# Kernel optimization log

Measured on AMD Instinct MI355X. Metric: run time of the kernel, lower is better.

## Reference

```python
import jax, jax.numpy as jnp
import numpy as np

UNITS = 1024
N_CLASS = 1024
D_IN = 1024


def setup_inputs() -> dict:
    key = jax.random.key(0)
    ks = jax.random.split(key, 12)
    B, T = 128, 256
    s_in = 1.0 / np.sqrt(D_IN)
    s_h = 1.0 / np.sqrt(UNITS)
    return {
        "x": jax.random.normal(ks[0], (B, T, D_IN), jnp.float32),
        "h0": jax.random.normal(ks[1], (B, UNITS), jnp.float32),
        "c0": jax.random.normal(ks[2], (B, UNITS), jnp.float32),
        "Wk": jax.random.normal(ks[3], (D_IN, 4 * UNITS), jnp.float32) * s_in,
        "bk": jnp.zeros((4 * UNITS,), jnp.float32),
        "Wr": jax.random.normal(ks[4], (UNITS, 4 * UNITS), jnp.float32) * s_h,
        "br": jnp.zeros((4 * UNITS,), jnp.float32),
        "alpha": jax.random.normal(ks[5], (1, 4 * UNITS), jnp.float32) * 0.1,
        "beta1": jax.random.normal(ks[6], (1, 4 * UNITS), jnp.float32) * 0.1,
        "beta2": jax.random.normal(ks[7], (1, 4 * UNITS), jnp.float32) * 0.1,
        "Wc": jax.random.normal(ks[8], (UNITS, N_CLASS), jnp.float32) * s_h,
        "bc": jnp.zeros((N_CLASS,), jnp.float32),
    }


def reference(x, h0, c0, Wk, bk, Wr, br, alpha, beta1, beta2, Wc, bc):
    # x: [B, T, D_in]; scan over time (steps) with MI-LSTM cell
    def step(carry, x_t):
        h, c = carry
        xp = x_t @ Wk + bk          # [B, 4U] input projection
        hp = h @ Wr + br            # [B, 4U] recurrent projection
        z = alpha * xp * hp + beta1 * xp + beta2 * hp  # multiplicative integration
        i, f, g, o = jnp.split(z, 4, axis=1)
        c_new = jnp.tanh(g) * jax.nn.sigmoid(i) + c * jax.nn.sigmoid(f)
        h_new = jnp.tanh(c_new) * jax.nn.sigmoid(o)
        return (h_new, c_new), None

    xs = jnp.transpose(x, (1, 0, 2))  # [T, B, D_in]
    (h, c), _ = jax.lax.scan(step, (h0, c0), xs)
    out = h @ Wc + bc  # [B, n_class]
    return out, h, c
```

## Files before the change

kernel.cpp:

```cpp
#include <hip/hip_runtime.h>


typedef unsigned short u16;
typedef __attribute__((ext_vector_type(8))) short short8;
typedef __attribute__((ext_vector_type(4))) float f32x4;

#define B_SZ   128
#define T_SZ   256
#define D_IN   1024
#define UNITS  1024
#define FOURU  4096

__device__ __forceinline__ float bf2f(u16 h) {
    return __uint_as_float(((unsigned int)h) << 16);
}
__device__ __forceinline__ u16 f2bf(float f) {
    unsigned int u = __float_as_uint(f);
    u += 0x7fffu + ((u >> 16) & 1u);
    return (u16)(u >> 16);
}
__device__ __forceinline__ float sigmoidf_(float x) {
    return 1.0f / (1.0f + __expf(-x));
}

__global__ __launch_bounds__(256) void transpose_cvt(
    const float* __restrict__ in, u16* __restrict__ out, int K, int N)
{
    __shared__ u16 t[32][33];
    int n0 = blockIdx.x * 32, k0 = blockIdx.y * 32;
    int c = threadIdx.x & 31, r = threadIdx.x >> 5;
    #pragma unroll
    for (int i = 0; i < 4; ++i) {
        int kk = r + i * 8;
        t[kk][c] = f2bf(in[(size_t)(k0 + kk) * N + n0 + c]);
    }
    __syncthreads();
    #pragma unroll
    for (int i = 0; i < 4; ++i) {
        int nn = r + i * 8;
        out[(size_t)(n0 + nn) * K + k0 + c] = t[c][nn];
    }
}

__global__ __launch_bounds__(256) void gemm_xp_chunk(
    const float* __restrict__ X, const u16* __restrict__ Bt,
    const float* __restrict__ bias, u16* __restrict__ Cc,
    int t0, int tcShift)
{
    __shared__ __align__(16) u16 As[128 * 40];
    __shared__ __align__(16) u16 Bs[128 * 40];
    int tid = threadIdx.x;
    int wave = tid >> 6, lane = tid & 63;
    int bm = blockIdx.x * 128;
    int bn = blockIdx.y * 128;
    int wm = (wave & 1) * 64, wn = (wave >> 1) * 64;
    int lm = lane & 15, lq = lane >> 4;
    int tcMask = (1 << tcShift) - 1;

    f32x4 acc[4][4] = {};

    for (int k0 = 0; k0 < D_IN; k0 += 32) {
        #pragma unroll
        for (int i = 0; i < 2; ++i) {
            int idx = tid + i * 256;
            int r = idx >> 2, q = idx & 3;
            int rowp = bm + r;
            int b = rowp >> tcShift;
            int tt = rowp & tcMask;
            const float* xs = &X[(size_t)(b * T_SZ + t0 + tt) * D_IN + k0 + q * 8];
            float4 f0 = *(const float4*)xs;
            float4 f1 = *(const float4*)(xs + 4);
            uint4 v;
            v.x = (unsigned)f2bf(f0.x) | ((unsigned)f2bf(f0.y) << 16);
            v.y = (unsigned)f2bf(f0.z) | ((unsigned)f2bf(f0.w) << 16);
            v.z = (unsigned)f2bf(f1.x) | ((unsigned)f2bf(f1.y) << 16);
            v.w = (unsigned)f2bf(f1.z) | ((unsigned)f2bf(f1.w) << 16);
            *(uint4*)&As[r * 40 + q * 8] = v;
            *(uint4*)&Bs[r * 40 + q * 8] =
                *(const uint4*)&Bt[(size_t)(bn + r) * D_IN + k0 + q * 8];
        }
        __syncthreads();
        short8 af[4], bf[4];
        #pragma unroll
        for (int t = 0; t < 4; ++t) {
            af[t] = *(const short8*)&As[(wm + t * 16 + lm) * 40 + lq * 8];
            bf[t] = *(const short8*)&Bs[(wn + t * 16 + lm) * 40 + lq * 8];
        }
        #pragma unroll
        for (int mt = 0; mt < 4; ++mt)
            #pragma unroll
            for (int nt = 0; nt < 4; ++nt)
                acc[mt][nt] = __builtin_amdgcn_mfma_f32_16x16x32_bf16(
                    af[mt], bf[nt], acc[mt][nt], 0, 0, 0);
        __syncthreads();
    }

    #pragma unroll
    for (int mt = 0; mt < 4; ++mt) {
        #pragma unroll
        for (int nt = 0; nt < 4; ++nt) {
            int col = bn + wn + nt * 16 + lm;
            float bv = bias[col];
            #pragma unroll
            for (int r = 0; r < 4; ++r) {
                int rowp = bm + wm + mt * 16 + lq * 4 + r;
                Cc[(size_t)rowp * FOURU + col] = f2bf(acc[mt][nt][r] + bv);
            }
        }
    }
}

__global__ __launch_bounds__(256) void milstm_chunk(
    const u16* __restrict__ XPc,
    const u16* __restrict__ WrT,
    const float* __restrict__ br,
    const float* __restrict__ alpha,
    const float* __restrict__ beta1,
    const float* __restrict__ beta2,
    const u16* __restrict__ h0bf,
    u16* __restrict__ hb0,
    u16* __restrict__ hb1,
    float* __restrict__ cbuf,
    unsigned* __restrict__ bar,
    int t0, int tc, int nbase)
{
    __shared__ __align__(16) u16 WrS[64 * 1032];
    __shared__ float zbuf[2][64][34];
    __shared__ float brS[64], alS[64], b1S[64], b2S[64];

    int tid = threadIdx.x;
    int wave = tid >> 6, lane = tid & 63;
    int lm = lane & 15, lq = lane >> 4;
    int mw = wave & 1, kh = wave >> 1;
    int bid = blockIdx.x;
    int grp = bid >> 6, grp0 = grp * 32;
    int u0 = (bid & 63) * 16;
    unsigned grpBase = (unsigned)grp * 256u;
    unsigned sub = ((unsigned)(bid & 63)) >> 4;

    for (int i = 0; i < 32; ++i) {
        int idx = i * 256 + tid;
        int l = idx >> 7, q = idx & 127;
        int n = ((l >> 4) << 10) + u0 + (l & 15);
        *(uint4*)&WrS[l * 1032 + q * 8] = *(const uint4*)&WrT[(size_t)n * 1024 + q * 8];
    }
    if (tid < 64) {
        int n = ((tid >> 4) << 10) + u0 + (tid & 15);
        brS[tid] = br[n]; alS[tid] = alpha[n];
        b1S[tid] = beta1[n]; b2S[tid] = beta2[n];
    }

    int rl = tid >> 3, j0 = (tid & 7) * 2;
    int bg = grp0 + rl;
    size_t cix = (size_t)bg * UNITS + u0 + j0;
    float cvl[2];
    { float2 c2 = *(const float2*)&cbuf[cix]; cvl[0] = c2.x; cvl[1] = c2.y; }
    __syncthreads();

    unsigned xpq[4];
    {
        const u16* xb = XPc + (size_t)(bg * tc) * FOURU + u0 + j0;
        #pragma unroll
        for (int g = 0; g < 4; ++g) xpq[g] = *(const unsigned*)(xb + (g << 10));
    }

    for (int s = 0; s < tc; ++s) {
        int t = t0 + s;
        const u16* hsrc = (t == 0) ? h0bf : ((t & 1) ? hb0 : hb1);
        u16* hdst = (t & 1) ? hb1 : hb0;

        unsigned long long* Ap = (unsigned long long*)
            &hsrc[(size_t)(grp0 + mw * 16 + lm) * UNITS + kh * 512 + lq * 8];
        unsigned long long aq[32];
        #pragma unroll
        for (int i = 0; i < 16; ++i) {
            aq[2 * i]     = __hip_atomic_load(Ap + i * 8,     __ATOMIC_RELAXED, __HIP_MEMORY_SCOPE_AGENT);
            aq[2 * i + 1] = __hip_atomic_load(Ap + i * 8 + 1, __ATOMIC_RELAXED, __HIP_MEMORY_SCOPE_AGENT);
        }

        const u16* Bl = &WrS[kh * 512 + lq * 8];
        f32x4 acc0 = {}, acc1 = {}, acc2 = {}, acc3 = {};
        #pragma unroll
        for (int i = 0; i < 16; ++i) {
            int k0 = i * 32;
            union { unsigned long long q[2]; short8 v; } a;
            a.q[0] = aq[2 * i]; a.q[1] = aq[2 * i + 1];
            short8 b0 = *(const short8*)&Bl[(0 * 16 + lm) * 1032 + k0];
            short8 b1 = *(const short8*)&Bl[(1 * 16 + lm) * 1032 + k0];
            short8 b2 = *(const short8*)&Bl[(2 * 16 + lm) * 1032 + k0];
            short8 b3 = *(const short8*)&Bl[(3 * 16 + lm) * 1032 + k0];
            acc0 = __builtin_amdgcn_mfma_f32_16x16x32_bf16(a.v, b0, acc0, 0, 0, 0);
            acc1 = __builtin_amdgcn_mfma_f32_16x16x32_bf16(a.v, b1, acc1, 0, 0, 0);
            acc2 = __builtin_amdgcn_mfma_f32_16x16x32_bf16(a.v, b2, acc2, 0, 0, 0);
            acc3 = __builtin_amdgcn_mfma_f32_16x16x32_bf16(a.v, b3, acc3, 0, 0, 0);
        }
        #pragma unroll
        for (int r = 0; r < 4; ++r) {
            int mrow = mw * 16 + lq * 4 + r;
            zbuf[kh][0 * 16 + lm][mrow] = acc0[r];
            zbuf[kh][1 * 16 + lm][mrow] = acc1[r];
            zbuf[kh][2 * 16 + lm][mrow] = acc2[r];
            zbuf[kh][3 * 16 + lm][mrow] = acc3[r];
        }
        __syncthreads();

        float hnew[2];
        #pragma unroll
        for (int jj = 0; jj < 2; ++jj) {
            float zz[4];
            #pragma unroll
            for (int g = 0; g < 4; ++g) {
                int l = g * 16 + j0 + jj;
                float hp = zbuf[0][l][rl] + zbuf[1][l][rl] + brS[l];
                float xp = bf2f((u16)(jj ? (xpq[g] >> 16) : (xpq[g] & 0xffffu)));
                zz[g] = alS[l] * xp * hp + b1S[l] * xp + b2S[l] * hp;
            }
            float cn = tanhf(zz[2]) * sigmoidf_(zz[0]) + cvl[jj] * sigmoidf_(zz[1]);
            cvl[jj] = cn;
            hnew[jj] = tanhf(cn) * sigmoidf_(zz[3]);
        }
        unsigned pk = (unsigned)f2bf(hnew[0]) | ((unsigned)f2bf(hnew[1]) << 16);
        __hip_atomic_store((unsigned*)&hdst[cix], pk,
                           __ATOMIC_RELAXED, __HIP_MEMORY_SCOPE_AGENT);

        if (s + 1 < tc) {
            {
                const u16* xb = XPc + (size_t)(bg * tc + s + 1) * FOURU + u0 + j0;
                #pragma unroll
                for (int g = 0; g < 4; ++g) xpq[g] = *(const unsigned*)(xb + (g << 10));
            }
            unsigned barId = (unsigned)(nbase + s + 1);
            __syncthreads();
            if (tid == 0) {
                unsigned old = __hip_atomic_fetch_add(&bar[grpBase + sub * 32u], 1u,
                                   __ATOMIC_RELAXED, __HIP_MEMORY_SCOPE_AGENT);
                if (old == 16u * barId - 1u)
                    __hip_atomic_fetch_add(&bar[grpBase + 128u], 1u,
                        __ATOMIC_RELAXED, __HIP_MEMORY_SCOPE_AGENT);
                while (__hip_atomic_load(&bar[grpBase + 128u],
                           __ATOMIC_RELAXED, __HIP_MEMORY_SCOPE_AGENT)
                       < 4u * barId)
                    __builtin_amdgcn_s_sleep(2);
            }
            __syncthreads();
        }
    }

    { float2 c2; c2.x = cvl[0]; c2.y = cvl[1]; *(float2*)&cbuf[cix] = c2; }
}

__global__ __launch_bounds__(256) void gemm_out(
    const u16* __restrict__ h, const u16* __restrict__ WcT,
    const float* __restrict__ bc, float* __restrict__ out)
{
    int tid = threadIdx.x;
    int wave = tid >> 6, lane = tid & 63;
    int bx = blockIdx.x;
    int row0 = (bx & 7) * 16;
    int n0 = (bx >> 3) * 64 + wave * 16;
    int lm = lane & 15, lq = lane >> 4;

    f32x4 acc = {};
    const u16* Arow = &h[(size_t)(row0 + lm) * UNITS];
    const u16* Brow = &WcT[(size_t)(n0 + lm) * UNITS];
    #pragma unroll 8
    for (int k0 = 0; k0 < UNITS; k0 += 32) {
        short8 a = *(const short8*)&Arow[k0 + lq * 8];
        short8 b = *(const short8*)&Brow[k0 + lq * 8];
        acc = __builtin_amdgcn_mfma_f32_16x16x32_bf16(a, b, acc, 0, 0, 0);
    }
    int col = n0 + lm;
    float bv = bc[col];
    #pragma unroll
    for (int r = 0; r < 4; ++r) {
        int row = row0 + lq * 4 + r;
        out[(size_t)row * 1024 + col] = acc[r] + bv;
    }
}

__global__ void cvt_f32_bf16(const float* __restrict__ in, u16* __restrict__ out, int n) {
    int i = blockIdx.x * 256 + threadIdx.x;
    if (i < n) out[i] = f2bf(in[i]);
}
__global__ void cvt_bf16_f32(const u16* __restrict__ in, float* __restrict__ out, int n) {
    int i = blockIdx.x * 256 + threadIdx.x;
    if (i < n) out[i] = bf2f(in[i]);
}
__global__ void copy_f32(const float* __restrict__ in, float* __restrict__ out, int n) {
    int i = blockIdx.x * 256 + threadIdx.x;
    if (i < n) out[i] = in[i];
}
__global__ void zero_u32(unsigned* __restrict__ p, int n) {
    int i = blockIdx.x * 256 + threadIdx.x;
    if (i < n) p[i] = 0u;
}

extern "C" void kernel_launch(void* const* d_in, const int* in_sizes, int n_in,
                              void* d_out, int out_size, void* d_ws, size_t ws_size,
                              hipStream_t stream)
{
    const float* x     = (const float*)d_in[0];
    const float* h0    = (const float*)d_in[1];
    const float* c0    = (const float*)d_in[2];
    const float* Wk    = (const float*)d_in[3];
    const float* bk    = (const float*)d_in[4];
    const float* Wr    = (const float*)d_in[5];
    const float* br    = (const float*)d_in[6];
    const float* alpha = (const float*)d_in[7];
    const float* beta1 = (const float*)d_in[8];
    const float* beta2 = (const float*)d_in[9];
    const float* Wc    = (const float*)d_in[10];
    const float* bc    = (const float*)d_in[11];
    float* out = (float*)d_out;

    char* p = (char*)d_ws;
    u16* h0bf = (u16*)p;  p += (size_t)B_SZ * UNITS * 2;
    u16* hb0  = (u16*)p;  p += (size_t)B_SZ * UNITS * 2;
    u16* hb1  = (u16*)p;  p += (size_t)B_SZ * UNITS * 2;
    float* cbuf = (float*)p; p += (size_t)B_SZ * UNITS * 4;
    unsigned* bar = (unsigned*)p; p += 4096;
    u16* WkT = (u16*)p;   p += (size_t)FOURU * D_IN * 2;
    u16* WrT = (u16*)p;   p += (size_t)FOURU * UNITS * 2;
    u16* WcT = (u16*)p;   p += (size_t)1024 * 1024 * 2;
    u16* XPc = (u16*)p;

    size_t fixedB = (size_t)(p - (char*)d_ws);
    int tc = 32, tcShift = 5;
    while (tc > 1 && fixedB + (size_t)B_SZ * tc * FOURU * 2 > ws_size) {
        tc >>= 1; tcShift -= 1;
    }

    transpose_cvt<<<dim3(FOURU / 32, D_IN / 32), 256, 0, stream>>>(Wk, WkT, D_IN, FOURU);
    transpose_cvt<<<dim3(FOURU / 32, UNITS / 32), 256, 0, stream>>>(Wr, WrT, UNITS, FOURU);
    transpose_cvt<<<dim3(1024 / 32, 1024 / 32), 256, 0, stream>>>(Wc, WcT, 1024, 1024);

    cvt_f32_bf16<<<(B_SZ * UNITS) / 256, 256, 0, stream>>>(h0, h0bf, B_SZ * UNITS);
    copy_f32<<<(B_SZ * UNITS) / 256, 256, 0, stream>>>(c0, cbuf, B_SZ * UNITS);
    zero_u32<<<4, 256, 0, stream>>>(bar, 1024);

    for (int t0 = 0; t0 < T_SZ; t0 += tc) {
        gemm_xp_chunk<<<dim3(tc, FOURU / 128), 256, 0, stream>>>(
            x, WkT, bk, XPc, t0, tcShift);
        int nbase = (t0 / tc) * (tc - 1);
        milstm_chunk<<<256, 256, 0, stream>>>(
            XPc, WrT, br, alpha, beta1, beta2, h0bf, hb0, hb1, cbuf, bar,
            t0, tc, nbase);
    }

    gemm_out<<<128, 256, 0, stream>>>(hb1, WcT, bc, out);
    cvt_bf16_f32<<<(B_SZ * UNITS) / 256, 256, 0, stream>>>(hb1, out + B_SZ * UNITS, B_SZ * UNITS);
    copy_f32<<<(B_SZ * UNITS) / 256, 256, 0, stream>>>(cbuf, out + 2 * B_SZ * UNITS, B_SZ * UNITS);
}
```

Baseline: 2.512 ms.

## Split recurrent blocks into two independent 16-row halves with per-half barriers

```diff
diff --git a/kernel.cpp b/kernel.cpp
--- a/kernel.cpp
+++ b/kernel.cpp
@@ -2,6 +2,7 @@
 
 
 typedef unsigned short u16;
+typedef unsigned long long u64t;
 typedef __attribute__((ext_vector_type(8))) short short8;
 typedef __attribute__((ext_vector_type(4))) float f32x4;
 
@@ -100,17 +101,19 @@
         #pragma unroll
         for (int nt = 0; nt < 4; ++nt) {
             int col = bn + wn + nt * 16 + lm;
+            int g = col >> 10, w = col & 1023;
+            int colp = ((w >> 4) << 6) + ((w & 15) << 2) + g;
             float bv = bias[col];
             #pragma unroll
             for (int r = 0; r < 4; ++r) {
                 int rowp = bm + wm + mt * 16 + lq * 4 + r;
-                Cc[(size_t)rowp * FOURU + col] = f2bf(acc[mt][nt][r] + bv);
-            }
-        }
-    }
-}
-
-__global__ __launch_bounds__(256) void milstm_chunk(
+                Cc[(size_t)rowp * FOURU + colp] = f2bf(acc[mt][nt][r] + bv);
+            }
+        }
+    }
+}
+
+__global__ __launch_bounds__(512) void milstm_chunk(
     const u16* __restrict__ XPc,
     const u16* __restrict__ WrT,
     const float* __restrict__ br,
@@ -124,129 +127,169 @@
     unsigned* __restrict__ bar,
     int t0, int tc, int nbase)
 {
-    __shared__ __align__(16) u16 WrS[64 * 1032];
-    __shared__ float zbuf[2][64][34];
+    __shared__ __align__(16) u16 WrS[64 * 1024];
+    __shared__ float zbuf[2][2][64][17];
     __shared__ float brS[64], alS[64], b1S[64], b2S[64];
+    __shared__ unsigned hsync[2];
+    __shared__ unsigned hflag[2];
 
     int tid = threadIdx.x;
-    int wave = tid >> 6, lane = tid & 63;
+    int bid = blockIdx.x;
+    int u_idx = bid & 63, gpair = bid >> 6;
+    int u0 = u_idx * 16;
+    int half = tid >> 8;
+    int x = tid & 255;
+    int kq = x >> 6;
+    int lane = tid & 63;
     int lm = lane & 15, lq = lane >> 4;
-    int mw = wave & 1, kh = wave >> 1;
-    int bid = blockIdx.x;
-    int grp = bid >> 6, grp0 = grp * 32;
-    int u0 = (bid & 63) * 16;
-    unsigned grpBase = (unsigned)grp * 256u;
-    unsigned sub = ((unsigned)(bid & 63)) >> 4;
-
-    for (int i = 0; i < 32; ++i) {
-        int idx = i * 256 + tid;
+    int grpRow0 = gpair * 32 + half * 16;
+    int group = gpair * 2 + half;
+    unsigned gBase = (unsigned)group * 256u;
+    unsigned sub = (unsigned)(u_idx >> 4);
+
+    #pragma unroll
+    for (int it = 0; it < 16; ++it) {
+        int idx = it * 512 + tid;
         int l = idx >> 7, q = idx & 127;
         int n = ((l >> 4) << 10) + u0 + (l & 15);
-        *(uint4*)&WrS[l * 1032 + q * 8] = *(const uint4*)&WrT[(size_t)n * 1024 + q * 8];
+        int byte = l * 2048 + ((q * 16) ^ ((l & 7) << 4));
+        *(uint4*)((char*)WrS + byte) = *(const uint4*)&WrT[(size_t)n * 1024 + q * 8];
     }
     if (tid < 64) {
         int n = ((tid >> 4) << 10) + u0 + (tid & 15);
         brS[tid] = br[n]; alS[tid] = alpha[n];
         b1S[tid] = beta1[n]; b2S[tid] = beta2[n];
     }
-
-    int rl = tid >> 3, j0 = (tid & 7) * 2;
-    int bg = grp0 + rl;
-    size_t cix = (size_t)bg * UNITS + u0 + j0;
-    float cvl[2];
-    { float2 c2 = *(const float2*)&cbuf[cix]; cvl[0] = c2.x; cvl[1] = c2.y; }
+    if (tid < 2) { hsync[tid] = 0u; hflag[tid] = 0u; }
+
+    int ej = x & 15, em = x >> 4;
+    int erow = grpRow0 + em;
+    size_t hixE = (size_t)erow * UNITS + u0 + ej;
+    float cv = cbuf[hixE];
+    u64t xq = *(const u64t*)&XPc[(size_t)(erow * tc) * FOURU + (u_idx << 6) + (ej << 2)];
     __syncthreads();
 
-    unsigned xpq[4];
-    {
-        const u16* xb = XPc + (size_t)(bg * tc) * FOURU + u0 + j0;
-        #pragma unroll
-        for (int g = 0; g < 4; ++g) xpq[g] = *(const unsigned*)(xb + (g << 10));
-    }
+    unsigned st = 0;
+    volatile unsigned* cnt = &hsync[half];
 
     for (int s = 0; s < tc; ++s) {
         int t = t0 + s;
         const u16* hsrc = (t == 0) ? h0bf : ((t & 1) ? hb0 : hb1);
         u16* hdst = (t & 1) ? hb1 : hb0;
 
-        unsigned long long* Ap = (unsigned long long*)
-            &hsrc[(size_t)(grp0 + mw * 16 + lm) * UNITS + kh * 512 + lq * 8];
-        unsigned long long aq[32];
-        #pragma unroll
-        for (int i = 0; i < 16; ++i) {
-            aq[2 * i]     = __hip_atomic_load(Ap + i * 8,     __ATOMIC_RELAXED, __HIP_MEMORY_SCOPE_AGENT);
-            aq[2 * i + 1] = __hip_atomic_load(Ap + i * 8 + 1, __ATOMIC_RELAXED, __HIP_MEMORY_SCOPE_AGENT);
-        }
-
-        const u16* Bl = &WrS[kh * 512 + lq * 8];
+        const u64t* A0 = (const u64t*)
+            &hsrc[(size_t)(grpRow0 + lm) * UNITS + kq * 256 + lq * 8];
+        u64t aq[16];
+        #pragma unroll
+        for (int i = 0; i < 8; ++i) {
+            aq[2 * i]     = __hip_atomic_load(A0 + i * 8,     __ATOMIC_RELAXED, __HIP_MEMORY_SCOPE_AGENT);
+            aq[2 * i + 1] = __hip_atomic_load(A0 + i * 8 + 1, __ATOMIC_RELAXED, __HIP_MEMORY_SCOPE_AGENT);
+        }
+
         f32x4 acc0 = {}, acc1 = {}, acc2 = {}, acc3 = {};
-        #pragma unroll
-        for (int i = 0; i < 16; ++i) {
-            int k0 = i * 32;
-            union { unsigned long long q[2]; short8 v; } a;
+        const char* Wb = (const char*)WrS;
+        int swz = (lm & 7) << 4;
+        #pragma unroll
+        for (int i = 0; i < 8; ++i) {
+            union { u64t q[2]; short8 v; } a;
             a.q[0] = aq[2 * i]; a.q[1] = aq[2 * i + 1];
-            short8 b0 = *(const short8*)&Bl[(0 * 16 + lm) * 1032 + k0];
-            short8 b1 = *(const short8*)&Bl[(1 * 16 + lm) * 1032 + k0];
-            short8 b2 = *(const short8*)&Bl[(2 * 16 + lm) * 1032 + k0];
-            short8 b3 = *(const short8*)&Bl[(3 * 16 + lm) * 1032 + k0];
+            int cb = ((kq * 512 + i * 64 + lq * 16) ^ swz);
+            short8 b0 = *(const short8*)(Wb + (0 * 16 + lm) * 2048 + cb);
+            short8 b1 = *(const short8*)(Wb + (1 * 16 + lm) * 2048 + cb);
+            short8 b2 = *(const short8*)(Wb + (2 * 16 + lm) * 2048 + cb);
+            short8 b3 = *(const short8*)(Wb + (3 * 16 + lm) * 2048 + cb);
             acc0 = __builtin_amdgcn_mfma_f32_16x16x32_bf16(a.v, b0, acc0, 0, 0, 0);
             acc1 = __builtin_amdgcn_mfma_f32_16x16x32_bf16(a.v, b1, acc1, 0, 0, 0);
             acc2 = __builtin_amdgcn_mfma_f32_16x16x32_bf16(a.v, b2, acc2, 0, 0, 0);
             acc3 = __builtin_amdgcn_mfma_f32_16x16x32_bf16(a.v, b3, acc3, 0, 0, 0);
         }
-        #pragma unroll
-        for (int r = 0; r < 4; ++r) {
-            int mrow = mw * 16 + lq * 4 + r;
-            zbuf[kh][0 * 16 + lm][mrow] = acc0[r];
-            zbuf[kh][1 * 16 + lm][mrow] = acc1[r];
-            zbuf[kh][2 * 16 + lm][mrow] = acc2[r];
-            zbuf[kh][3 * 16 + lm][mrow] = acc3[r];
-        }
-        __syncthreads();
-
-        float hnew[2];
-        #pragma unroll
-        for (int jj = 0; jj < 2; ++jj) {
+
+        if (kq < 2) {
+            #pragma unroll
+            for (int r = 0; r < 4; ++r) {
+                int m = lq * 4 + r;
+                zbuf[half][kq][0 * 16 + lm][m] = acc0[r];
+                zbuf[half][kq][1 * 16 + lm][m] = acc1[r];
+                zbuf[half][kq][2 * 16 + lm][m] = acc2[r];
+                zbuf[half][kq][3 * 16 + lm][m] = acc3[r];
+            }
+        }
+        {
+            st += 4;
+            asm volatile("s_waitcnt lgkmcnt(0)" ::: "memory");
+            if (lane == 0)
+                __hip_atomic_fetch_add((unsigned*)cnt, 1u, __ATOMIC_RELAXED, __HIP_MEMORY_SCOPE_WORKGROUP);
+            while (__hip_atomic_load((unsigned*)cnt, __ATOMIC_RELAXED, __HIP_MEMORY_SCOPE_WORKGROUP) < st)
+                __builtin_amdgcn_s_sleep(1);
+        }
+        if (kq >= 2) {
+            int L = kq - 2;
+            #pragma unroll
+            for (int r = 0; r < 4; ++r) {
+                int m = lq * 4 + r;
+                zbuf[half][L][0 * 16 + lm][m] += acc0[r];
+                zbuf[half][L][1 * 16 + lm][m] += acc1[r];
+                zbuf[half][L][2 * 16 + lm][m] += acc2[r];
+                zbuf[half][L][3 * 16 + lm][m] += acc3[r];
+            }
+        }
+        {
+            st += 4;
+            asm volatile("s_waitcnt lgkmcnt(0)" ::: "memory");
+            if (lane == 0)
+                __hip_atomic_fetch_add((unsigned*)cnt, 1u, __ATOMIC_RELAXED, __HIP_MEMORY_SCOPE_WORKGROUP);
+            while (__hip_atomic_load((unsigned*)cnt, __ATOMIC_RELAXED, __HIP_MEMORY_SCOPE_WORKGROUP) < st)
+                __builtin_amdgcn_s_sleep(1);
+        }
+
+        {
             float zz[4];
             #pragma unroll
             for (int g = 0; g < 4; ++g) {
-                int l = g * 16 + j0 + jj;
-                float hp = zbuf[0][l][rl] + zbuf[1][l][rl] + brS[l];
-                float xp = bf2f((u16)(jj ? (xpq[g] >> 16) : (xpq[g] & 0xffffu)));
+                int l = g * 16 + ej;
+                float hp = zbuf[half][0][l][em] + zbuf[half][1][l][em] + brS[l];
+                float xp = bf2f((u16)(xq >> (16 * g)));
                 zz[g] = alS[l] * xp * hp + b1S[l] * xp + b2S[l] * hp;
             }
-            float cn = tanhf(zz[2]) * sigmoidf_(zz[0]) + cvl[jj] * sigmoidf_(zz[1]);
-            cvl[jj] = cn;
-            hnew[jj] = tanhf(cn) * sigmoidf_(zz[3]);
-        }
-        unsigned pk = (unsigned)f2bf(hnew[0]) | ((unsigned)f2bf(hnew[1]) << 16);
-        __hip_atomic_store((unsigned*)&hdst[cix], pk,
-                           __ATOMIC_RELAXED, __HIP_MEMORY_SCOPE_AGENT);
+            float cn = tanhf(zz[2]) * sigmoidf_(zz[0]) + cv * sigmoidf_(zz[1]);
+            cv = cn;
+            u16 hv = f2bf(tanhf(cn) * sigmoidf_(zz[3]));
+            __hip_atomic_store(&hdst[hixE], hv, __ATOMIC_RELAXED, __HIP_MEMORY_SCOPE_AGENT);
+        }
 
         if (s + 1 < tc) {
-            {
-                const u16* xb = XPc + (size_t)(bg * tc + s + 1) * FOURU + u0 + j0;
-                #pragma unroll
-                for (int g = 0; g < 4; ++g) xpq[g] = *(const unsigned*)(xb + (g << 10));
-            }
-            unsigned barId = (unsigned)(nbase + s + 1);
-            __syncthreads();
-            if (tid == 0) {
-                unsigned old = __hip_atomic_fetch_add(&bar[grpBase + sub * 32u], 1u,
+            asm volatile("s_waitcnt vmcnt(0)" ::: "memory");
+            xq = *(const u64t*)&XPc[(size_t)(erow * tc + s + 1) * FOURU
+                                    + (u_idx << 6) + (ej << 2)];
+
+            st += 4;
+            asm volatile("s_waitcnt lgkmcnt(0)" ::: "memory");
+            if (lane == 0)
+                __hip_atomic_fetch_add((unsigned*)cnt, 1u, __ATOMIC_RELAXED, __HIP_MEMORY_SCOPE_WORKGROUP);
+            while (__hip_atomic_load((unsigned*)cnt, __ATOMIC_RELAXED, __HIP_MEMORY_SCOPE_WORKGROUP) < st)
+                __builtin_amdgcn_s_sleep(1);
+
+            if (x == 0) {
+                unsigned barId = (unsigned)(nbase + s + 1);
+                unsigned old = __hip_atomic_fetch_add(&bar[gBase + sub * 32u], 1u,
                                    __ATOMIC_RELAXED, __HIP_MEMORY_SCOPE_AGENT);
                 if (old == 16u * barId - 1u)
-                    __hip_atomic_fetch_add(&bar[grpBase + 128u], 1u,
+                    __hip_atomic_fetch_add(&bar[gBase + 128u], 1u,
                         __ATOMIC_RELAXED, __HIP_MEMORY_SCOPE_AGENT);
-                while (__hip_atomic_load(&bar[grpBase + 128u],
+                while (__hip_atomic_load(&bar[gBase + 128u],
                            __ATOMIC_RELAXED, __HIP_MEMORY_SCOPE_AGENT)
                        < 4u * barId)
                     __builtin_amdgcn_s_sleep(2);
-            }
-            __syncthreads();
-        }
-    }
-
-    { float2 c2; c2.x = cvl[0]; c2.y = cvl[1]; *(float2*)&cbuf[cix] = c2; }
+                __hip_atomic_store(&hflag[half], (unsigned)(s + 1),
+                                   __ATOMIC_RELAXED, __HIP_MEMORY_SCOPE_WORKGROUP);
+            }
+            while (__hip_atomic_load(&hflag[half], __ATOMIC_RELAXED, __HIP_MEMORY_SCOPE_WORKGROUP)
+                   < (unsigned)(s + 1))
+                __builtin_amdgcn_s_sleep(1);
+        }
+    }
+
+    cbuf[hixE] = cv;
 }
 
 __global__ __launch_bounds__(256) void gemm_out(
@@ -318,7 +361,7 @@
     u16* hb0  = (u16*)p;  p += (size_t)B_SZ * UNITS * 2;
     u16* hb1  = (u16*)p;  p += (size_t)B_SZ * UNITS * 2;
     float* cbuf = (float*)p; p += (size_t)B_SZ * UNITS * 4;
-    unsigned* bar = (unsigned*)p; p += 4096;
+    unsigned* bar = (unsigned*)p; p += 8 * 256 * 4;
     u16* WkT = (u16*)p;   p += (size_t)FOURU * D_IN * 2;
     u16* WrT = (u16*)p;   p += (size_t)FOURU * UNITS * 2;
     u16* WcT = (u16*)p;   p += (size_t)1024 * 1024 * 2;
@@ -336,13 +379,13 @@
 
     cvt_f32_bf16<<<(B_SZ * UNITS) / 256, 256, 0, stream>>>(h0, h0bf, B_SZ * UNITS);
     copy_f32<<<(B_SZ * UNITS) / 256, 256, 0, stream>>>(c0, cbuf, B_SZ * UNITS);
-    zero_u32<<<4, 256, 0, stream>>>(bar, 1024);
+    zero_u32<<<8, 256, 0, stream>>>(bar, 2048);
 
     for (int t0 = 0; t0 < T_SZ; t0 += tc) {
         gemm_xp_chunk<<<dim3(tc, FOURU / 128), 256, 0, stream>>>(
             x, WkT, bk, XPc, t0, tcShift);
         int nbase = (t0 / tc) * (tc - 1);
-        milstm_chunk<<<256, 256, 0, stream>>>(
+        milstm_chunk<<<256, 512, 0, stream>>>(
             XPc, WrT, br, alpha, beta1, beta2, h0bf, hb0, hb1, cbuf, bar,
             t0, tc, nbase);
     }
```

Measured after the change: 2.750 ms. 9.5% more time.

## Keep recurrent weights in registers and repartition MI-LSTM cells per block

Applied to the files above, without the earlier changes.

```diff
diff --git a/kernel.cpp b/kernel.cpp
--- a/kernel.cpp
+++ b/kernel.cpp
@@ -2,6 +2,7 @@
 
 
 typedef unsigned short u16;
+typedef unsigned long long u64t;
 typedef __attribute__((ext_vector_type(8))) short short8;
 typedef __attribute__((ext_vector_type(4))) float f32x4;
 
@@ -100,17 +101,18 @@
         #pragma unroll
         for (int nt = 0; nt < 4; ++nt) {
             int col = bn + wn + nt * 16 + lm;
+            int colp = ((col & 1023) << 2) | (col >> 10);
             float bv = bias[col];
             #pragma unroll
             for (int r = 0; r < 4; ++r) {
                 int rowp = bm + wm + mt * 16 + lq * 4 + r;
-                Cc[(size_t)rowp * FOURU + col] = f2bf(acc[mt][nt][r] + bv);
-            }
-        }
-    }
-}
-
-__global__ __launch_bounds__(256) void milstm_chunk(
+                Cc[(size_t)rowp * FOURU + colp] = f2bf(acc[mt][nt][r] + bv);
+            }
+        }
+    }
+}
+
+__global__ __launch_bounds__(512) void milstm_chunk(
     const u16* __restrict__ XPc,
     const u16* __restrict__ WrT,
     const float* __restrict__ br,
@@ -122,131 +124,117 @@
     u16* __restrict__ hb1,
     float* __restrict__ cbuf,
     unsigned* __restrict__ bar,
-    int t0, int tc, int nbase)
-{
-    __shared__ __align__(16) u16 WrS[64 * 1032];
-    __shared__ float zbuf[2][64][34];
-    __shared__ float brS[64], alS[64], b1S[64], b2S[64];
+    int t0, int tc, int tcShift, int nbase)
+{
+    __shared__ __align__(16) u16 hS[16 * 1024];
+    __shared__ __align__(16) float zb[2][128][20];
+    __shared__ float brS[128], alS[128], b1S[128], b2S[128];
 
     int tid = threadIdx.x;
     int wave = tid >> 6, lane = tid & 63;
     int lm = lane & 15, lq = lane >> 4;
-    int mw = wave & 1, kh = wave >> 1;
+    int kh = wave >> 2, nq = wave & 3;
     int bid = blockIdx.x;
-    int grp = bid >> 6, grp0 = grp * 32;
-    int u0 = (bid & 63) * 16;
-    unsigned grpBase = (unsigned)grp * 256u;
-    unsigned sub = ((unsigned)(bid & 63)) >> 4;
-
-    for (int i = 0; i < 32; ++i) {
-        int idx = i * 256 + tid;
-        int l = idx >> 7, q = idx & 127;
-        int n = ((l >> 4) << 10) + u0 + (l & 15);
-        *(uint4*)&WrS[l * 1032 + q * 8] = *(const uint4*)&WrT[(size_t)n * 1024 + q * 8];
-    }
-    if (tid < 64) {
-        int n = ((tid >> 4) << 10) + u0 + (tid & 15);
+    int grp = bid >> 5, cb = bid & 31;
+    int row0 = grp * 16;
+    int ubase = cb * 32;
+    unsigned gOff = (unsigned)grp * 64u;
+
+    if (tid < 128) {
+        int n = ((tid & 3) << 10) + ubase + (tid >> 2);
         brS[tid] = br[n]; alS[tid] = alpha[n];
         b1S[tid] = beta1[n]; b2S[tid] = beta2[n];
     }
-
-    int rl = tid >> 3, j0 = (tid & 7) * 2;
-    int bg = grp0 + rl;
-    size_t cix = (size_t)bg * UNITS + u0 + j0;
-    float cvl[2];
-    { float2 c2 = *(const float2*)&cbuf[cix]; cvl[0] = c2.x; cvl[1] = c2.y; }
-    __syncthreads();
-
-    unsigned xpq[4];
-    {
-        const u16* xb = XPc + (size_t)(bg * tc) * FOURU + u0 + j0;
-        #pragma unroll
-        for (int g = 0; g < 4; ++g) xpq[g] = *(const unsigned*)(xb + (g << 10));
-    }
+    short8 Breg[32];
+    #pragma unroll
+    for (int j = 0; j < 16; ++j) {
+        #pragma unroll
+        for (int nt = 0; nt < 2; ++nt) {
+            int c = nq * 32 + nt * 16 + lm;
+            int n = ((c & 3) << 10) + ubase + (c >> 2);
+            int k = kh * 512 + j * 32 + lq * 8;
+            Breg[j * 2 + nt] = *(const short8*)&WrT[(size_t)n * 1024 + k];
+        }
+    }
+    int erow = tid & 15, eul = tid >> 4;
+    size_t hix = (size_t)(row0 + erow) * UNITS + ubase + eul;
+    float cv = cbuf[hix];
+    u64t xq = *(const u64t*)&XPc[((size_t)((row0 + erow) << tcShift) + 0) * FOURU
+                                 + (size_t)(ubase + eul) * 4];
+    int sr = tid >> 5, sc = tid & 31;
+    unsigned swzS = (unsigned)((sr & 7) << 4);
 
     for (int s = 0; s < tc; ++s) {
         int t = t0 + s;
         const u16* hsrc = (t == 0) ? h0bf : ((t & 1) ? hb0 : hb1);
         u16* hdst = (t & 1) ? hb1 : hb0;
 
-        unsigned long long* Ap = (unsigned long long*)
-            &hsrc[(size_t)(grp0 + mw * 16 + lm) * UNITS + kh * 512 + lq * 8];
-        unsigned long long aq[32];
-        #pragma unroll
-        for (int i = 0; i < 16; ++i) {
-            aq[2 * i]     = __hip_atomic_load(Ap + i * 8,     __ATOMIC_RELAXED, __HIP_MEMORY_SCOPE_AGENT);
-            aq[2 * i + 1] = __hip_atomic_load(Ap + i * 8 + 1, __ATOMIC_RELAXED, __HIP_MEMORY_SCOPE_AGENT);
-        }
-
-        const u16* Bl = &WrS[kh * 512 + lq * 8];
-        f32x4 acc0 = {}, acc1 = {}, acc2 = {}, acc3 = {};
-        #pragma unroll
-        for (int i = 0; i < 16; ++i) {
-            int k0 = i * 32;
-            union { unsigned long long q[2]; short8 v; } a;
-            a.q[0] = aq[2 * i]; a.q[1] = aq[2 * i + 1];
-            short8 b0 = *(const short8*)&Bl[(0 * 16 + lm) * 1032 + k0];
-            short8 b1 = *(const short8*)&Bl[(1 * 16 + lm) * 1032 + k0];
-            short8 b2 = *(const short8*)&Bl[(2 * 16 + lm) * 1032 + k0];
-            short8 b3 = *(const short8*)&Bl[(3 * 16 + lm) * 1032 + k0];
-            acc0 = __builtin_amdgcn_mfma_f32_16x16x32_bf16(a.v, b0, acc0, 0, 0, 0);
-            acc1 = __builtin_amdgcn_mfma_f32_16x16x32_bf16(a.v, b1, acc1, 0, 0, 0);
-            acc2 = __builtin_amdgcn_mfma_f32_16x16x32_bf16(a.v, b2, acc2, 0, 0, 0);
-            acc3 = __builtin_amdgcn_mfma_f32_16x16x32_bf16(a.v, b3, acc3, 0, 0, 0);
-        }
-        #pragma unroll
-        for (int r = 0; r < 4; ++r) {
-            int mrow = mw * 16 + lq * 4 + r;
-            zbuf[kh][0 * 16 + lm][mrow] = acc0[r];
-            zbuf[kh][1 * 16 + lm][mrow] = acc1[r];
-            zbuf[kh][2 * 16 + lm][mrow] = acc2[r];
-            zbuf[kh][3 * 16 + lm][mrow] = acc3[r];
+        {
+            const u64t* hp8 = (const u64t*)&hsrc[(size_t)(row0 + sr) * UNITS] + sc * 8;
+            u64t aq[8];
+            #pragma unroll
+            for (int i = 0; i < 8; ++i)
+                aq[i] = __hip_atomic_load(hp8 + i, __ATOMIC_RELAXED, __HIP_MEMORY_SCOPE_AGENT);
+            char* dst = (char*)hS + sr * 2048;
+            int base = sc * 64;
+            #pragma unroll
+            for (int q = 0; q < 4; ++q) {
+                uint4 v;
+                v.x = (unsigned)aq[2 * q];     v.y = (unsigned)(aq[2 * q] >> 32);
+                v.z = (unsigned)aq[2 * q + 1]; v.w = (unsigned)(aq[2 * q + 1] >> 32);
+                *(uint4*)(dst + (((unsigned)(base + q * 16)) ^ swzS)) = v;
+            }
         }
         __syncthreads();
 
-        float hnew[2];
-        #pragma unroll
-        for (int jj = 0; jj < 2; ++jj) {
+        f32x4 acc0 = {}, acc1 = {};
+        {
+            unsigned swzA = (unsigned)((lm & 7) << 4);
+            const char* hb = (const char*)hS + lm * 2048;
+            #pragma unroll
+            for (int j = 0; j < 16; ++j) {
+                unsigned koff = (unsigned)(kh * 1024 + j * 64 + lq * 16);
+                short8 a = *(const short8*)(hb + (koff ^ swzA));
+                acc0 = __builtin_amdgcn_mfma_f32_16x16x32_bf16(a, Breg[j * 2],     acc0, 0, 0, 0);
+                acc1 = __builtin_amdgcn_mfma_f32_16x16x32_bf16(a, Breg[j * 2 + 1], acc1, 0, 0, 0);
+            }
+        }
+        *(f32x4*)&zb[kh][nq * 32 + lm][lq * 4]      = acc0;
+        *(f32x4*)&zb[kh][nq * 32 + 16 + lm][lq * 4] = acc1;
+        __syncthreads();
+
+        {
             float zz[4];
             #pragma unroll
             for (int g = 0; g < 4; ++g) {
-                int l = g * 16 + j0 + jj;
-                float hp = zbuf[0][l][rl] + zbuf[1][l][rl] + brS[l];
-                float xp = bf2f((u16)(jj ? (xpq[g] >> 16) : (xpq[g] & 0xffffu)));
-                zz[g] = alS[l] * xp * hp + b1S[l] * xp + b2S[l] * hp;
-            }
-            float cn = tanhf(zz[2]) * sigmoidf_(zz[0]) + cvl[jj] * sigmoidf_(zz[1]);
-            cvl[jj] = cn;
-            hnew[jj] = tanhf(cn) * sigmoidf_(zz[3]);
-        }
-        unsigned pk = (unsigned)f2bf(hnew[0]) | ((unsigned)f2bf(hnew[1]) << 16);
-        __hip_atomic_store((unsigned*)&hdst[cix], pk,
-                           __ATOMIC_RELAXED, __HIP_MEMORY_SCOPE_AGENT);
-
+                int c = eul * 4 + g;
+                float hp = zb[0][c][erow] + zb[1][c][erow] + brS[c];
+                float xp = bf2f((u16)(xq >> (16 * g)));
+                zz[g] = alS[c] * xp * hp + b1S[c] * xp + b2S[c] * hp;
+            }
+            float cn = tanhf(zz[2]) * sigmoidf_(zz[0]) + cv * sigmoidf_(zz[1]);
+            cv = cn;
+            u16 hv = f2bf(tanhf(cn) * sigmoidf_(zz[3]));
+            __hip_atomic_store(&hdst[hix], hv, __ATOMIC_RELAXED, __HIP_MEMORY_SCOPE_AGENT);
+        }
         if (s + 1 < tc) {
-            {
-                const u16* xb = XPc + (size_t)(bg * tc + s + 1) * FOURU + u0 + j0;
-                #pragma unroll
-                for (int g = 0; g < 4; ++g) xpq[g] = *(const unsigned*)(xb + (g << 10));
-            }
-            unsigned barId = (unsigned)(nbase + s + 1);
+            xq = *(const u64t*)&XPc[((size_t)((row0 + erow) << tcShift) + s + 1) * FOURU
+                                     + (size_t)(ubase + eul) * 4];
             __syncthreads();
             if (tid == 0) {
-                unsigned old = __hip_atomic_fetch_add(&bar[grpBase + sub * 32u], 1u,
-                                   __ATOMIC_RELAXED, __HIP_MEMORY_SCOPE_AGENT);
-                if (old == 16u * barId - 1u)
-                    __hip_atomic_fetch_add(&bar[grpBase + 128u], 1u,
-                        __ATOMIC_RELAXED, __HIP_MEMORY_SCOPE_AGENT);
-                while (__hip_atomic_load(&bar[grpBase + 128u],
+                unsigned barId = (unsigned)(nbase + s + 1);
+                __hip_atomic_fetch_add(&bar[gOff], 1u,
+                    __ATOMIC_RELAXED, __HIP_MEMORY_SCOPE_AGENT);
+                while (__hip_atomic_load(&bar[gOff],
                            __ATOMIC_RELAXED, __HIP_MEMORY_SCOPE_AGENT)
-                       < 4u * barId)
-                    __builtin_amdgcn_s_sleep(2);
+                       < 32u * barId)
+                    __builtin_amdgcn_s_sleep(1);
             }
             __syncthreads();
         }
     }
 
-    { float2 c2; c2.x = cvl[0]; c2.y = cvl[1]; *(float2*)&cbuf[cix] = c2; }
+    cbuf[hix] = cv;
 }
 
 __global__ __launch_bounds__(256) void gemm_out(
@@ -318,7 +306,7 @@
     u16* hb0  = (u16*)p;  p += (size_t)B_SZ * UNITS * 2;
     u16* hb1  = (u16*)p;  p += (size_t)B_SZ * UNITS * 2;
     float* cbuf = (float*)p; p += (size_t)B_SZ * UNITS * 4;
-    unsigned* bar = (unsigned*)p; p += 4096;
+    unsigned* bar = (unsigned*)p; p += 8 * 64 * 4;
     u16* WkT = (u16*)p;   p += (size_t)FOURU * D_IN * 2;
     u16* WrT = (u16*)p;   p += (size_t)FOURU * UNITS * 2;
     u16* WcT = (u16*)p;   p += (size_t)1024 * 1024 * 2;
@@ -336,15 +324,15 @@
 
     cvt_f32_bf16<<<(B_SZ * UNITS) / 256, 256, 0, stream>>>(h0, h0bf, B_SZ * UNITS);
     copy_f32<<<(B_SZ * UNITS) / 256, 256, 0, stream>>>(c0, cbuf, B_SZ * UNITS);
-    zero_u32<<<4, 256, 0, stream>>>(bar, 1024);
+    zero_u32<<<2, 256, 0, stream>>>(bar, 512);
 
     for (int t0 = 0; t0 < T_SZ; t0 += tc) {
         gemm_xp_chunk<<<dim3(tc, FOURU / 128), 256, 0, stream>>>(
             x, WkT, bk, XPc, t0, tcShift);
         int nbase = (t0 / tc) * (tc - 1);
-        milstm_chunk<<<256, 256, 0, stream>>>(
+        milstm_chunk<<<256, 512, 0, stream>>>(
             XPc, WrT, br, alpha, beta1, beta2, h0bf, hb0, hb1, cbuf, bar,
-            t0, tc, nbase);
+            t0, tc, tcShift, nbase);
     }
 
     gemm_out<<<128, 256, 0, stream>>>(hb1, WcT, bc, out);
```

Result: faster. 2.248 ms (-10.5%).
